# Performance work log

Measured on AMD Instinct MI355X. Metric: run time of the kernel, lower is better.

## Reference

```python
import jax, jax.numpy as jnp
import numpy as np

N = 50000      # nodes
E = 800000     # edges (avg degree 16)
IN = 128       # in_feats
HID = 32       # hidden_feats per head
H = 4          # num_heads
NEG_SLOPE = 0.2


def setup_inputs() -> dict:
    key = jax.random.key(0)
    ks = jax.random.split(key, 13)
    x = jax.random.normal(ks[0], (N, IN), jnp.float32)
    src = jax.random.randint(ks[1], (E,), 0, N, jnp.int32)
    dst = jax.random.randint(ks[2], (E,), 0, N, jnp.int32)

    def lin(k, fi, fo):
        return jax.random.normal(k, (fi, fo), jnp.float32) * (1.0 / np.sqrt(fi))

    # conv1: IN -> H*HID
    W1 = lin(ks[3], IN, H * HID)
    al1 = jax.random.normal(ks[4], (H, HID), jnp.float32) * 0.1
    ar1 = jax.random.normal(ks[5], (H, HID), jnp.float32) * 0.1
    b1 = jnp.zeros((H, HID), jnp.float32)
    # conv2: H*HID -> H*HID
    W2 = lin(ks[6], H * HID, H * HID)
    al2 = jax.random.normal(ks[7], (H, HID), jnp.float32) * 0.1
    ar2 = jax.random.normal(ks[8], (H, HID), jnp.float32) * 0.1
    b2 = jnp.zeros((H, HID), jnp.float32)
    # fc: HID -> 1
    fcW = lin(ks[9], HID, 1)
    fcb = jnp.zeros((1,), jnp.float32)
    return {"x": x, "src": src, "dst": dst,
            "W1": W1, "al1": al1, "ar1": ar1, "b1": b1,
            "W2": W2, "al2": al2, "ar2": ar2, "b2": b2,
            "fcW": fcW, "fcb": fcb}


def gat_conv(x, src, dst, W, al, ar, b):
    # x: [N, F_in] -> feat: [N, H, HID]
    feat = (x @ W).reshape(N, H, HID)
    el = jnp.sum(feat * al, axis=-1)            # [N, H]
    er = jnp.sum(feat * ar, axis=-1)            # [N, H]
    e = jax.nn.leaky_relu(el[src] + er[dst], NEG_SLOPE)  # [E, H]
    # segment softmax over incoming edges of each dst node
    m = jax.ops.segment_max(e, dst, num_segments=N)      # [N, H]
    ex = jnp.exp(e - m[dst])                              # [E, H]
    denom = jax.ops.segment_sum(ex, dst, num_segments=N)  # [N, H]
    alpha = ex / denom[dst]                                # [E, H]
    msg = feat[src] * alpha[:, :, None]                    # [E, H, HID]
    out = jax.ops.segment_sum(msg, dst, num_segments=N)   # [N, H, HID]
    return out + b[None, :, :]


def reference(x, src, dst, W1, al1, ar1, b1, W2, al2, ar2, b2, fcW, fcb):
    h = gat_conv(x, src, dst, W1, al1, ar1, b1).reshape(N, H * HID)
    h = jax.nn.relu(h)
    # dropout(0.5) is identity in eval mode
    h = gat_conv(h, src, dst, W2, al2, ar2, b2).mean(axis=1)  # [N, HID]
    return h @ fcW + fcb                                       # [N, 1]
```

## Files before the change

### kernel.cpp

```cpp
#include <hip/hip_runtime.h>
#include <hip/hip_fp16.h>

#define LEAK 0.2f
#define CAP 64
#define CS 16

static __device__ inline int swz(int c, int j) {
    int qb = j >> 3, r = j & 7;
    return c * 144 + qb * 8 + (qb >> 2) * 4 + r;
}
static __device__ inline unsigned q4(float4 v, float is) {
    int x0 = __float2int_rn(v.x * is) + 128; x0 = min(max(x0, 0), 255);
    int x1 = __float2int_rn(v.y * is) + 128; x1 = min(max(x1, 0), 255);
    int x2 = __float2int_rn(v.z * is) + 128; x2 = min(max(x2, 0), 255);
    int x3 = __float2int_rn(v.w * is) + 128; x3 = min(max(x3, 0), 255);
    return (unsigned)x0 | ((unsigned)x1 << 8) | ((unsigned)x2 << 16) | ((unsigned)x3 << 24);
}

__global__ __launch_bounds__(256) void k0(
    int* __restrict__ cnt,
    const int* __restrict__ src, const int* __restrict__ dst,
    unsigned* __restrict__ pk,
    const float* __restrict__ W2, const float* __restrict__ al2,
    const float* __restrict__ ar2, const float* __restrict__ fcW,
    const float* __restrict__ b2, float* __restrict__ WfT,
    float* __restrict__ bc, int N, int E, int zb, int pkb) {
    const int b = blockIdx.x;
    const int t = threadIdx.x;
    if (b < zb) {
        int i = b * 256 + t;
        if (i < N * (CS / 4)) ((int4*)cnt)[i] = make_int4(0, 0, 0, 0);
        return;
    }
    if (b < zb + pkb) {
        int i = (b - zb) * 256 + t;
        int e0 = i * 4;
        if (e0 + 3 < E) {
            int4 d = ((const int4*)dst)[i];
            int4 s = ((const int4*)src)[i];
            ((int4*)pk)[i] = make_int4((d.x << 16) | s.x, (d.y << 16) | s.y,
                                       (d.z << 16) | s.z, (d.w << 16) | s.w);
        } else if (e0 < E) {
            for (int e = e0; e < E; e++) pk[e] = ((unsigned)dst[e] << 16) | (unsigned)src[e];
        }
        return;
    }
    int idx = (b - zb - pkb) * 256 + t;
    if (idx < 1536) {
        int c = idx >> 7, k = idx & 127;
        int h = c & 3, sel = c >> 2;
        const float* vec = (sel == 0) ? (al2 + 32 * h)
                         : (sel == 1) ? (ar2 + 32 * h) : fcW;
        float s = 0.f;
#pragma unroll 8
        for (int m = 0; m < 32; m++) s += W2[k * 128 + 32 * h + m] * vec[m];
        WfT[c * 128 + k] = s;
    } else if (idx < 1540) {
        int h = idx - 1536;
        float s = 0.f;
        for (int m = 0; m < 32; m++) s += b2[h * 32 + m] * fcW[m];
        bc[h] = s;
    }
}

__global__ __launch_bounds__(256, 4) void k_eg(
    const float* __restrict__ X, const float* __restrict__ W,
    const float* __restrict__ al, const float* __restrict__ ar,
    float2* __restrict__ elsc2, float* __restrict__ er_nh,
    unsigned* __restrict__ fq8,
    const unsigned* __restrict__ pk,
    int* __restrict__ cnt, unsigned short* __restrict__ ell,
    int N, int E, int R, int GO, int T) {
    __shared__ float sW[32 * 128];
    __shared__ float sXT[32 * 64];
    const int b = blockIdx.x;
    const int t = threadIdx.x;
    const int o = b >> 3;
    const int g0 = (o * GO) / T;
    const bool isGemm = ((o + 1) * GO) / T > g0;

    if (!isGemm) {
        const int part = b & 7;
        const int rank = o - g0;
        const int S = (N + 7) >> 3;
        const int lo = part * S;
        const int hi = (lo + S < N) ? (lo + S) : N;
        const int per = (E + R - 1) / R;
        const int e0 = rank * per;
        const int e1 = (e0 + per < E) ? (e0 + per) : E;
        int e = e0 + t;
        for (; e + 768 < e1; e += 1024) {
            unsigned p0 = pk[e];       unsigned p1 = pk[e + 256];
            unsigned p2 = pk[e + 512]; unsigned p3 = pk[e + 768];
            int d0 = (int)(p0 >> 16), d1 = (int)(p1 >> 16);
            int d2 = (int)(p2 >> 16), d3 = (int)(p3 >> 16);
            if (d0 >= lo && d0 < hi) {
                int pos = atomicAdd(&cnt[d0 * CS], 1);
                if (pos < CAP) ell[(size_t)d0 * CAP + pos] = (unsigned short)(p0 & 0xffffu);
            }
            if (d1 >= lo && d1 < hi) {
                int pos = atomicAdd(&cnt[d1 * CS], 1);
                if (pos < CAP) ell[(size_t)d1 * CAP + pos] = (unsigned short)(p1 & 0xffffu);
            }
            if (d2 >= lo && d2 < hi) {
                int pos = atomicAdd(&cnt[d2 * CS], 1);
                if (pos < CAP) ell[(size_t)d2 * CAP + pos] = (unsigned short)(p2 & 0xffffu);
            }
            if (d3 >= lo && d3 < hi) {
                int pos = atomicAdd(&cnt[d3 * CS], 1);
                if (pos < CAP) ell[(size_t)d3 * CAP + pos] = (unsigned short)(p3 & 0xffffu);
            }
        }
        for (; e < e1; e += 256) {
            unsigned p = pk[e];
            int d = (int)(p >> 16);
            if (d >= lo && d < hi) {
                int pos = atomicAdd(&cnt[d * CS], 1);
                if (pos < CAP) ell[(size_t)d * CAP + pos] = (unsigned short)(p & 0xffffu);
            }
        }
        return;
    }

    const int tile = g0 * 8 + (b & 7);
    const int r0 = tile * 64;
    if (r0 >= N) return;
    const int tx = t & 15;
    const int ty = t >> 4;
    const float4* X4 = (const float4*)X;
    const float4* W4 = (const float4*)W;
    float4* sW4 = (float4*)sW;
    const float4* sXT4 = (const float4*)sXT;

    float4 acc[4][2];
#pragma unroll
    for (int r = 0; r < 4; r++) {
        acc[r][0] = make_float4(0.f, 0.f, 0.f, 0.f);
        acc[r][1] = make_float4(0.f, 0.f, 0.f, 0.f);
    }
    for (int ks = 0; ks < 4; ++ks) {
        if (ks) __syncthreads();
#pragma unroll
        for (int i = 0; i < 4; i++) {
            int idx = i * 256 + t;
            sW4[idx] = W4[1024 * ks + idx];
        }
#pragma unroll
        for (int i = 0; i < 2; i++) {
            int idx = i * 256 + t;
            int row = idx >> 3;
            int kq = idx & 7;
            float4 v = make_float4(0.f, 0.f, 0.f, 0.f);
            if (r0 + row < N) v = X4[(size_t)(r0 + row) * 32 + ks * 8 + kq];
            int sc = ((row >> 2) ^ kq) * 4 + (row & 3);
            sXT[(4 * kq + 0) * 64 + sc] = v.x;
            sXT[(4 * kq + 1) * 64 + sc] = v.y;
            sXT[(4 * kq + 2) * 64 + sc] = v.z;
            sXT[(4 * kq + 3) * 64 + sc] = v.w;
        }
        __syncthreads();
#pragma unroll 4
        for (int k = 0; k < 32; k++) {
            float4 w0 = sW4[k * 32 + tx];
            float4 w1 = sW4[k * 32 + 16 + tx];
            float4 x0 = sXT4[k * 16 + (ty ^ (k >> 2))];
            float xs[4] = {x0.x, x0.y, x0.z, x0.w};
#pragma unroll
            for (int r = 0; r < 4; r++) {
                acc[r][0].x += xs[r] * w0.x; acc[r][0].y += xs[r] * w0.y;
                acc[r][0].z += xs[r] * w0.z; acc[r][0].w += xs[r] * w0.w;
                acc[r][1].x += xs[r] * w1.x; acc[r][1].y += xs[r] * w1.y;
                acc[r][1].z += xs[r] * w1.z; acc[r][1].w += xs[r] * w1.w;
            }
        }
    }
    const float4* al4p = (const float4*)al;
    const float4* ar4p = (const float4*)ar;
    float4 alA = al4p[tx], alB = al4p[16 + tx];
    float4 arA = ar4p[tx], arB = ar4p[16 + tx];
#pragma unroll
    for (int r = 0; r < 4; r++) {
        int row = r0 + ty * 4 + r;
        bool ok = row < N;
        float4 a0 = acc[r][0], a1 = acc[r][1];
        float m = fmaxf(fmaxf(fmaxf(fabsf(a0.x), fabsf(a0.y)),
                              fmaxf(fabsf(a0.z), fabsf(a0.w))),
                        fmaxf(fmaxf(fabsf(a1.x), fabsf(a1.y)),
                              fmaxf(fabsf(a1.z), fabsf(a1.w))));
#pragma unroll
        for (int off = 1; off < 16; off <<= 1) m = fmaxf(m, __shfl_xor(m, off));
        float scale = m * (1.f / 127.f);
        float is = (m > 0.f) ? (127.f / m) : 0.f;
        if (ok) {
            fq8[(size_t)row * 32 + tx] = q4(a0, is);
            fq8[(size_t)row * 32 + 16 + tx] = q4(a1, is);
        }
        float elA = a0.x * alA.x + a0.y * alA.y + a0.z * alA.z + a0.w * alA.w;
        float erA = a0.x * arA.x + a0.y * arA.y + a0.z * arA.z + a0.w * arA.w;
        float elB = a1.x * alB.x + a1.y * alB.y + a1.z * alB.z + a1.w * alB.w;
        float erB = a1.x * arB.x + a1.y * arB.y + a1.z * arB.z + a1.w * arB.w;
#pragma unroll
        for (int off = 1; off < 8; off <<= 1) {
            elA += __shfl_xor(elA, off); erA += __shfl_xor(erA, off);
            elB += __shfl_xor(elB, off); erB += __shfl_xor(erB, off);
        }
        if (ok && tx == 0) {
            elsc2[row * 4 + 0] = make_float2(elA, scale);
            elsc2[row * 4 + 2] = make_float2(elB, scale);
            er_nh[row * 4 + 0] = erA;
            er_nh[row * 4 + 2] = erB;
        }
        if (ok && tx == 8) {
            elsc2[row * 4 + 1] = make_float2(elA, scale);
            elsc2[row * 4 + 3] = make_float2(elB, scale);
            er_nh[row * 4 + 1] = erA;
            er_nh[row * 4 + 3] = erB;
        }
    }
}

__global__ __launch_bounds__(256) void k_agg1P(
    const unsigned* __restrict__ fq8, const float2* __restrict__ elsc2,
    const float* __restrict__ er_nh, const unsigned short* __restrict__ ell,
    const int* __restrict__ cnt, const float* __restrict__ b1,
    const float* __restrict__ WfT, float2* __restrict__ Pag,
    float* __restrict__ er2, int N) {
    __shared__ float sWf[12 * 144];
    for (int i = threadIdx.x; i < 1536; i += 256)
        sWf[swz(i >> 7, i & 127)] = WfT[i];
    __syncthreads();
    const int wave = threadIdx.x >> 6, lane = threadIdx.x & 63;
    const int nsub = lane >> 4, q = lane & 15, h = q >> 2;
    const int wbase = q * 8 + (q >> 2) * 4;
    const uint2* fq2 = (const uint2*)fq8;

    const int n = blockIdx.x * 16 + wave * 4 + nsub;
    const bool nok = n < N;
    const int nc = nok ? n : (N - 1);
    int deg = nok ? cnt[nc * CS] : 0; if (deg > CAP) deg = CAP;
    float er = nok ? er_nh[nc * 4 + h] : 0.f;
    const unsigned short* row = ell + (size_t)nc * CAP;
    uint2 rv = ((const uint2*)row)[q];

    float acc[8] = {0.f, 0.f, 0.f, 0.f, 0.f, 0.f, 0.f, 0.f};
    float den = 0.f, wss = 0.f;
    for (int j0 = 0; j0 < deg; j0 += 8) {
        int sv[8]; float2 esv[8]; uint2 fv[8];
#pragma unroll
        for (int v = 0; v < 8; v++) {
            int wrd = __shfl((int)((v & 2) ? rv.y : rv.x),
                             (lane & 48) | ((j0 >> 2) + (v >> 2)));
            int s = (v & 1) ? ((wrd >> 16) & 0xffff) : (wrd & 0xffff);
            sv[v] = (j0 + v < deg) ? s : 0;
        }
#pragma unroll
        for (int v = 0; v < 8; v++) esv[v] = elsc2[sv[v] * 4 + h];
#pragma unroll
        for (int v = 0; v < 8; v++) fv[v] = fq2[(size_t)sv[v] * 16 + q];
#pragma unroll
        for (int v = 0; v < 8; v++) {
            bool valid = (j0 + v) < deg;
            float e = esv[v].x + er;
            e = fmaxf(e, LEAK * e);
            float w = valid ? __expf(e) : 0.f;
            float ws = w * esv[v].y;
            unsigned ua = fv[v].x, ub = fv[v].y;
            acc[0] += ws * (float)(ua & 0xff);
            acc[1] += ws * (float)((ua >> 8) & 0xff);
            acc[2] += ws * (float)((ua >> 16) & 0xff);
            acc[3] += ws * (float)(ua >> 24);
            acc[4] += ws * (float)(ub & 0xff);
            acc[5] += ws * (float)((ub >> 8) & 0xff);
            acc[6] += ws * (float)((ub >> 16) & 0xff);
            acc[7] += ws * (float)(ub >> 24);
            den += w; wss += ws;
        }
    }
    float inv = (den > 0.f) ? (1.f / den) : 0.f;
    float off128 = 128.f * wss;
    float4 b1a = ((const float4*)b1)[q * 2];
    float4 b1b = ((const float4*)b1)[q * 2 + 1];
    float hv[8];
    hv[0] = fmaxf((acc[0] - off128) * inv + b1a.x, 0.f);
    hv[1] = fmaxf((acc[1] - off128) * inv + b1a.y, 0.f);
    hv[2] = fmaxf((acc[2] - off128) * inv + b1a.z, 0.f);
    hv[3] = fmaxf((acc[3] - off128) * inv + b1a.w, 0.f);
    hv[4] = fmaxf((acc[4] - off128) * inv + b1b.x, 0.f);
    hv[5] = fmaxf((acc[5] - off128) * inv + b1b.y, 0.f);
    hv[6] = fmaxf((acc[6] - off128) * inv + b1b.z, 0.f);
    hv[7] = fmaxf((acc[7] - off128) * inv + b1b.w, 0.f);
    float p[12];
#pragma unroll
    for (int c = 0; c < 12; c++) {
        const float* wr = sWf + c * 144 + wbase;
        float4 wa = *(const float4*)wr;
        float4 wb = *(const float4*)(wr + 4);
        p[c] = hv[0] * wa.x + hv[1] * wa.y + hv[2] * wa.z + hv[3] * wa.w
             + hv[4] * wb.x + hv[5] * wb.y + hv[6] * wb.z + hv[7] * wb.w;
    }
#pragma unroll
    for (int off = 1; off < 16; off <<= 1) {
#pragma unroll
        for (int c = 0; c < 12; c++) p[c] += __shfl_xor(p[c], off);
    }
    if (nok) {
        if (q < 4) Pag[(size_t)n * 4 + q] = make_float2(p[q], p[8 + q]);
        else if (q < 8) er2[(size_t)n * 4 + (q - 4)] = p[q];
    }
}

__global__ __launch_bounds__(256) void k_agg2(
    const float2* __restrict__ Pag, const float* __restrict__ er2,
    const unsigned short* __restrict__ ell, const int* __restrict__ cnt,
    const float* __restrict__ bc, const float* __restrict__ fcb,
    float* __restrict__ out, int N) {
    int idx = blockIdx.x * 256 + threadIdx.x;
    int n = idx >> 2, h = idx & 3;
    if (n >= N) return;
    int deg = cnt[n * CS]; if (deg > CAP) deg = CAP;
    float er = er2[(size_t)n * 4 + h];
    const uint4* row4 = (const uint4*)(ell + (size_t)n * CAP);
    uint4 rv[8];
#pragma unroll
    for (int i = 0; i < 8; i++) rv[i] = row4[i];

    float num = 0.f, den = 0.f;
#pragma unroll
    for (int b8 = 0; b8 < 8; ++b8) {
        int j0 = b8 * 8;
        if (j0 >= deg) break;
        int sv[8];
#pragma unroll
        for (int v = 0; v < 8; v++) {
            unsigned wrd = ((v >> 1) == 0) ? rv[b8].x
                         : ((v >> 1) == 1) ? rv[b8].y
                         : ((v >> 1) == 2) ? rv[b8].z : rv[b8].w;
            int s = (v & 1) ? (int)(wrd >> 16) : (int)(wrd & 0xffffu);
            sv[v] = (j0 + v < deg) ? s : 0;
        }
        float2 g[8];
#pragma unroll
        for (int v = 0; v < 8; v++) g[v] = Pag[(size_t)sv[v] * 4 + h];
#pragma unroll
        for (int v = 0; v < 8; v++) {
            if (j0 + v < deg) {
                float e = g[v].x + er; e = fmaxf(e, LEAK * e);
                float w = __expf(e);
                num += w * g[v].y; den += w;
            }
        }
    }
    float r = (den > 0.f) ? (num / den) : 0.f;
    r += bc[h];
    r += __shfl_xor(r, 1);
    r += __shfl_xor(r, 2);
    if (h == 0) out[n] = 0.25f * r + fcb[0];
}

extern "C" void kernel_launch(void* const* d_in, const int* in_sizes, int n_in,
                              void* d_out, int out_size, void* d_ws, size_t ws_size,
                              hipStream_t stream) {
    const float* x   = (const float*)d_in[0];
    const int* src   = (const int*)d_in[1];
    const int* dst   = (const int*)d_in[2];
    const float* W1  = (const float*)d_in[3];
    const float* al1 = (const float*)d_in[4];
    const float* ar1 = (const float*)d_in[5];
    const float* b1  = (const float*)d_in[6];
    const float* W2  = (const float*)d_in[7];
    const float* al2 = (const float*)d_in[8];
    const float* ar2 = (const float*)d_in[9];
    const float* b2  = (const float*)d_in[10];
    const float* fcW = (const float*)d_in[11];
    const float* fcb = (const float*)d_in[12];
    float* out = (float*)d_out;

    const int N = in_sizes[0] / 128;
    const int E = in_sizes[1];

    char* w = (char*)d_ws;
    size_t off = 0;
    auto alloc = [&](size_t bytes) {
        void* p = w + off;
        off = (off + bytes + 255) & ~(size_t)255;
        return p;
    };
    unsigned* fq8  = (unsigned*)alloc((size_t)N * 32 * 4);
    float2* elsc2  = (float2*)alloc((size_t)N * 4 * 8);
    float* er_nh   = (float*)alloc((size_t)N * 4 * 4);
    float2* Pag    = (float2*)alloc((size_t)N * 4 * 8);
    float* er2     = (float*)alloc((size_t)N * 4 * 4);
    float* WfT     = (float*)alloc((size_t)(12 * 128 + 4) * 4);
    float* bc      = WfT + 12 * 128;
    int* cnt       = (int*)alloc((size_t)N * CS * 4);
    unsigned short* ell = (unsigned short*)alloc((size_t)N * CAP * 2);
    unsigned* pk   = (unsigned*)alloc((size_t)E * 4);

    const int zb = (N * (CS / 4) + 255) / 256;
    const int pkb = (E / 4 + 255) / 256;
    const int gtiles = (N + 63) / 64;
    const int R = 256;
    const int GO = (gtiles + 7) / 8;
    const int T = R + GO;

    k0<<<zb + pkb + 8, 256, 0, stream>>>(
        cnt, src, dst, pk, W2, al2, ar2, fcW, b2, WfT, bc, N, E, zb, pkb);
    k_eg<<<8 * T, 256, 0, stream>>>(
        x, W1, al1, ar1, elsc2, er_nh, fq8,
        pk, cnt, ell, N, E, R, GO, T);
    k_agg1P<<<(N + 15) / 16, 256, 0, stream>>>(
        fq8, elsc2, er_nh, ell, cnt, b1, WfT, Pag, er2, N);
    k_agg2<<<(N * 4 + 255) / 256, 256, 0, stream>>>(
        Pag, er2, ell, cnt, bc, fcb, out, N);
}
```

Measured before the change: 186.5 us.

## Split layer-1 aggregation into two head-pair passes with 4-byte feature gathers

The layer-1 aggregation kernel now runs its edge loop twice. Each pass covers a pair of heads and each lane gathers a single 32-bit word of quantized features instead of an 8-byte uint2. This makes each gather across a 16-lane group one contiguous 64-byte segment per source node, and it cuts accumulator registers. In exchange the edge-index shuffles and the attention-logit loads and exp are done twice. The shared-memory weight indexing is remapped to match the new feature-to-lane assignment.

```diff
diff --git a/kernel.cpp b/kernel.cpp
--- a/kernel.cpp
+++ b/kernel.cpp
@@ -230,82 +230,77 @@
         sWf[swz(i >> 7, i & 127)] = WfT[i];
     __syncthreads();
     const int wave = threadIdx.x >> 6, lane = threadIdx.x & 63;
-    const int nsub = lane >> 4, q = lane & 15, h = q >> 2;
-    const int wbase = q * 8 + (q >> 2) * 4;
-    const uint2* fq2 = (const uint2*)fq8;
+    const int nsub = lane >> 4, q = lane & 15;
 
     const int n = blockIdx.x * 16 + wave * 4 + nsub;
     const bool nok = n < N;
     const int nc = nok ? n : (N - 1);
     int deg = nok ? cnt[nc * CS] : 0; if (deg > CAP) deg = CAP;
-    float er = nok ? er_nh[nc * 4 + h] : 0.f;
     const unsigned short* row = ell + (size_t)nc * CAP;
     uint2 rv = ((const uint2*)row)[q];
 
-    float acc[8] = {0.f, 0.f, 0.f, 0.f, 0.f, 0.f, 0.f, 0.f};
-    float den = 0.f, wss = 0.f;
-    for (int j0 = 0; j0 < deg; j0 += 8) {
-        int sv[8]; float2 esv[8]; uint2 fv[8];
-#pragma unroll
-        for (int v = 0; v < 8; v++) {
-            int wrd = __shfl((int)((v & 2) ? rv.y : rv.x),
-                             (lane & 48) | ((j0 >> 2) + (v >> 2)));
-            int s = (v & 1) ? ((wrd >> 16) & 0xffff) : (wrd & 0xffff);
-            sv[v] = (j0 + v < deg) ? s : 0;
-        }
-#pragma unroll
-        for (int v = 0; v < 8; v++) esv[v] = elsc2[sv[v] * 4 + h];
-#pragma unroll
-        for (int v = 0; v < 8; v++) fv[v] = fq2[(size_t)sv[v] * 16 + q];
-#pragma unroll
-        for (int v = 0; v < 8; v++) {
-            bool valid = (j0 + v) < deg;
-            float e = esv[v].x + er;
-            e = fmaxf(e, LEAK * e);
-            float w = valid ? __expf(e) : 0.f;
-            float ws = w * esv[v].y;
-            unsigned ua = fv[v].x, ub = fv[v].y;
-            acc[0] += ws * (float)(ua & 0xff);
-            acc[1] += ws * (float)((ua >> 8) & 0xff);
-            acc[2] += ws * (float)((ua >> 16) & 0xff);
-            acc[3] += ws * (float)(ua >> 24);
-            acc[4] += ws * (float)(ub & 0xff);
-            acc[5] += ws * (float)((ub >> 8) & 0xff);
-            acc[6] += ws * (float)((ub >> 16) & 0xff);
-            acc[7] += ws * (float)(ub >> 24);
-            den += w; wss += ws;
-        }
-    }
-    float inv = (den > 0.f) ? (1.f / den) : 0.f;
-    float off128 = 128.f * wss;
-    float4 b1a = ((const float4*)b1)[q * 2];
-    float4 b1b = ((const float4*)b1)[q * 2 + 1];
     float hv[8];
-    hv[0] = fmaxf((acc[0] - off128) * inv + b1a.x, 0.f);
-    hv[1] = fmaxf((acc[1] - off128) * inv + b1a.y, 0.f);
-    hv[2] = fmaxf((acc[2] - off128) * inv + b1a.z, 0.f);
-    hv[3] = fmaxf((acc[3] - off128) * inv + b1a.w, 0.f);
-    hv[4] = fmaxf((acc[4] - off128) * inv + b1b.x, 0.f);
-    hv[5] = fmaxf((acc[5] - off128) * inv + b1b.y, 0.f);
-    hv[6] = fmaxf((acc[6] - off128) * inv + b1b.z, 0.f);
-    hv[7] = fmaxf((acc[7] - off128) * inv + b1b.w, 0.f);
-    float p[12];
+#pragma unroll
+    for (int p = 0; p < 2; p++) {
+        const int h = p * 2 + (q >> 3);
+        const float er = nok ? er_nh[nc * 4 + h] : 0.f;
+        float acc0 = 0.f, acc1 = 0.f, acc2 = 0.f, acc3 = 0.f;
+        float den = 0.f, wss = 0.f;
+        for (int j0 = 0; j0 < deg; j0 += 8) {
+            int sv[8]; float2 esv[8]; unsigned fv[8];
+#pragma unroll
+            for (int v = 0; v < 8; v++) {
+                int wrd = __shfl((int)((v & 2) ? rv.y : rv.x),
+                                 (lane & 48) | ((j0 >> 2) + (v >> 2)));
+                int s = (v & 1) ? ((wrd >> 16) & 0xffff) : (wrd & 0xffff);
+                sv[v] = (j0 + v < deg) ? s : 0;
+            }
+#pragma unroll
+            for (int v = 0; v < 8; v++) esv[v] = elsc2[sv[v] * 4 + h];
+#pragma unroll
+            for (int v = 0; v < 8; v++)
+                fv[v] = fq8[(size_t)sv[v] * 32 + p * 16 + q];
+#pragma unroll
+            for (int v = 0; v < 8; v++) {
+                bool valid = (j0 + v) < deg;
+                float e = esv[v].x + er;
+                e = fmaxf(e, LEAK * e);
+                float w = valid ? __expf(e) : 0.f;
+                float ws = w * esv[v].y;
+                unsigned ua = fv[v];
+                acc0 += ws * (float)(ua & 0xff);
+                acc1 += ws * (float)((ua >> 8) & 0xff);
+                acc2 += ws * (float)((ua >> 16) & 0xff);
+                acc3 += ws * (float)(ua >> 24);
+                den += w; wss += ws;
+            }
+        }
+        float inv = (den > 0.f) ? (1.f / den) : 0.f;
+        float off128 = 128.f * wss;
+        float4 bb = ((const float4*)b1)[p * 16 + q];
+        hv[p * 4 + 0] = fmaxf((acc0 - off128) * inv + bb.x, 0.f);
+        hv[p * 4 + 1] = fmaxf((acc1 - off128) * inv + bb.y, 0.f);
+        hv[p * 4 + 2] = fmaxf((acc2 - off128) * inv + bb.z, 0.f);
+        hv[p * 4 + 3] = fmaxf((acc3 - off128) * inv + bb.w, 0.f);
+    }
+    const int w0 = (q >> 1) * 8 + (q >> 3) * 4 + (q & 1) * 4;
+    float pr[12];
 #pragma unroll
     for (int c = 0; c < 12; c++) {
-        const float* wr = sWf + c * 144 + wbase;
-        float4 wa = *(const float4*)wr;
-        float4 wb = *(const float4*)(wr + 4);
-        p[c] = hv[0] * wa.x + hv[1] * wa.y + hv[2] * wa.z + hv[3] * wa.w
-             + hv[4] * wb.x + hv[5] * wb.y + hv[6] * wb.z + hv[7] * wb.w;
+        const float* wr = sWf + c * 144;
+        float4 wa = *(const float4*)(wr + w0);
+        float4 wb = *(const float4*)(wr + w0 + 72);
+        pr[c] = hv[0] * wa.x + hv[1] * wa.y + hv[2] * wa.z + hv[3] * wa.w
+              + hv[4] * wb.x + hv[5] * wb.y + hv[6] * wb.z + hv[7] * wb.w;
     }
 #pragma unroll
     for (int off = 1; off < 16; off <<= 1) {
 #pragma unroll
-        for (int c = 0; c < 12; c++) p[c] += __shfl_xor(p[c], off);
+        for (int c = 0; c < 12; c++) pr[c] += __shfl_xor(pr[c], off);
     }
     if (nok) {
-        if (q < 4) Pag[(size_t)n * 4 + q] = make_float2(p[q], p[8 + q]);
-        else if (q < 8) er2[(size_t)n * 4 + (q - 4)] = p[q];
+        if (q < 4) Pag[(size_t)n * 4 + q] = make_float2(pr[q], pr[8 + q]);
+        else if (q < 8) er2[(size_t)n * 4 + (q - 4)] = pr[q];
     }
 }
 
```

Result: slower. 195.0 us (+4.5%).
